# Performance work log

Hardware: AMD Instinct MI355X
Metric: run time of the kernel (lower is better)

Reference implementation:

```python
import jax, jax.numpy as jnp
import numpy as np

B, M, H, E = 1, 2048, 16, 128
D = H * E          # 2048, model dim
C = 4 * D          # 8192, FFN dim
F = E
G = D
J = D


def setup_inputs() -> dict:
    key = jax.random.key(0)
    k_in, k_wv, k_wk, k_wq, k_wz, k_ffa, k_ffb = jax.random.split(key, 7)
    scale = 0.01
    return {
        "I_in": jax.random.normal(k_in, (B, M, D), dtype=jnp.float32),
        "WV": jax.random.normal(k_wv, (H, E, D), dtype=jnp.float32) * scale,
        "WK": jax.random.normal(k_wk, (H, E, D), dtype=jnp.float32) * scale,
        "WQ": jax.random.normal(k_wq, (H, E, D), dtype=jnp.float32) * scale,
        "WZ": jax.random.normal(k_wz, (H, F, G), dtype=jnp.float32) * scale,
        "WFFA": jax.random.normal(k_ffa, (G, C), dtype=jnp.float32) * scale,
        "WFFB": jax.random.normal(k_ffb, (C, J), dtype=jnp.float32) * scale,
    }


def reference(I_in, WV, WK, WQ, WZ, WFFA, WFFB):
    # QKV projections: [B,M,D] x [H,E,D] -> [B,M,H,E]
    V = jnp.einsum('bmd,hed->bmhe', I_in, WV)
    K = jnp.einsum('bmd,hed->bmhe', I_in, WK)
    Q = jnp.einsum('bmd,hed->bmhe', I_in, WQ)
    # Attention scores [B,M,P,H]; NOTE: no 1/sqrt(E) scaling in the original.
    QK = jnp.einsum('bmhe,bphe->bmph', Q, K)
    # Softmax over keys (p axis = 2), matching torch.softmax(QK, dim=2)
    QK_softmax = jax.nn.softmax(QK, axis=2)
    # Attention output [B,M,H,E]
    AV = jnp.einsum('bmph,bphe->bmhe', QK_softmax, V)
    # Output projection [B,M,G]
    Z = jnp.einsum('bmhf,hfg->bmg', AV, WZ)
    # FFN (no nonlinearity in the original workload)
    FFA = jnp.einsum('bmg,gc->bmc', Z, WFFA)
    FFB = jnp.einsum('bmc,cj->bmj', FFA, WFFB)
    return FFB
```

## Files before the change

### kernel.cpp

```cpp
#include <hip/hip_runtime.h>
#include <hip/hip_bf16.h>
#include <math.h>


typedef __bf16 bf16_t;
typedef __bf16 bf16x8 __attribute__((ext_vector_type(8)));
typedef float  f32x4  __attribute__((ext_vector_type(4)));

#define AS1 __attribute__((address_space(1)))
#define AS3 __attribute__((address_space(3)))

__device__ __forceinline__ void load16_lds(const bf16_t* g, bf16_t* l) {
    __builtin_amdgcn_global_load_lds((AS1 void*)g, (AS3 void*)l, 16, 0, 0);
}

__device__ __forceinline__ void stageA_half(const bf16_t* __restrict__ Ab, int lda,
                                            int k0, int h, bf16_t* slot,
                                            int w, int lane)
{
    #pragma unroll
    for (int j = 0; j < 2; ++j) {
        const int prw = j * 64 + w * 8;
        const int p   = prw + (lane >> 3);
        const int lr  = (p >> 6) * 128 + h * 64 + (p & 63);
        const int lc  = (lane & 7) ^ (p & 7);
        load16_lds(Ab + (long long)lr * lda + k0 + lc * 8, slot + prw * 64);
    }
}
__device__ __forceinline__ void stageB_half(const bf16_t* __restrict__ Bb, int ldb,
                                            int k0, int h, bf16_t* slot,
                                            int w, int lane)
{
    #pragma unroll
    for (int j = 0; j < 2; ++j) {
        const int prw = j * 64 + w * 8;
        const int p   = prw + (lane >> 3);
        const int lr  = (p >> 5) * 64 + h * 32 + (p & 31);
        const int lc  = (lane & 7) ^ (p & 7);
        load16_lds(Bb + (long long)lr * ldb + k0 + lc * 8, slot + prw * 64);
    }
}

#define LOADAF(DST, SL)                                                        \
  _Pragma("unroll") for (int ks = 0; ks < 2; ++ks)                             \
  _Pragma("unroll") for (int mi = 0; mi < 4; ++mi)                             \
      DST[ks][mi] = *(const bf16x8*)&(SL)[(wm * 64 + mi * 16 + c15) * 64 +     \
                      (((ks * 4 + q4) ^ (c15 & 7)) * 8)];

#define LOADBV(DST, SL)                                                        \
  _Pragma("unroll") for (int ks = 0; ks < 2; ++ks)                             \
  _Pragma("unroll") for (int nj = 0; nj < 2; ++nj)                             \
      DST[ks][nj] = *(const bf16x8*)&(SL)[(wn * 32 + nj * 16 + c15) * 64 +     \
                      (((ks * 4 + q4) ^ (c15 & 7)) * 8)];

#define MFMA8(R0, C0)                                                          \
  _Pragma("unroll") for (int ks = 0; ks < 2; ++ks)                             \
  _Pragma("unroll") for (int mi = 0; mi < 4; ++mi)                             \
  _Pragma("unroll") for (int nj = 0; nj < 2; ++nj)                             \
      acc[(R0) + mi][(C0) + nj] = __builtin_amdgcn_mfma_f32_16x16x32_bf16(     \
          af[ks][mi], bv[ks][nj], acc[(R0) + mi][(C0) + nj], 0, 0, 0);

#define VMW(N)  asm volatile("s_waitcnt vmcnt(" #N ")" ::: "memory")
#define BAR()   __builtin_amdgcn_s_barrier()

#define PHASE8(RDS, STGS, GATE, R0, C0)                                        \
  RDS;                                                                         \
  STGS;                                                                        \
  GATE;                                                                        \
  __builtin_amdgcn_s_barrier();                                                \
  asm volatile("s_waitcnt lgkmcnt(0)" ::: "memory");                           \
  __builtin_amdgcn_sched_barrier(0);                                           \
  __builtin_amdgcn_s_setprio(1);                                               \
  MFMA8(R0, C0);                                                               \
  __builtin_amdgcn_s_setprio(0);                                               \
  __builtin_amdgcn_s_barrier();

template<typename TOUT>
__global__ __launch_bounds__(512, 2)
void gemm256p_bt(const bf16_t* __restrict__ A, const bf16_t* __restrict__ B,
                 TOUT* __restrict__ Cc, int Kdim,
                 int lda, int ldb, int ldc,
                 long long ab, long long bb, long long cb,
                 int ct_z, bf16_t* __restrict__ ctc, int ldct)
{
    __shared__ __attribute__((aligned(16))) bf16_t As4[4][128 * 64];
    __shared__ __attribute__((aligned(16))) bf16_t Bs4[4][128 * 64];

    const int z = blockIdx.z;
    A  += (long long)z * ab;
    B  += (long long)z * bb;
    Cc += (long long)z * cb;

    const int bm = blockIdx.y * 256;
    const int bn = blockIdx.x * 256;
    const int t = threadIdx.x, lane = t & 63, w = t >> 6;
    const int wm = w >> 2, wn = w & 3;
    const int q4 = lane >> 4, c15 = lane & 15;

    const bf16_t* Ab = A + (long long)bm * lda;
    const bf16_t* Bb = B + (long long)bn * ldb;

    f32x4  acc[8][4] = {};
    bf16x8 af[2][4];
    bf16x8 bv[2][2];

    stageB_half(Bb, ldb, 0,  0, Bs4[0], w, lane);
    stageA_half(Ab, lda, 0,  1, As4[1], w, lane);
    stageA_half(Ab, lda, 0,  0, As4[0], w, lane);
    stageB_half(Bb, ldb, 0,  1, Bs4[1], w, lane);
    stageB_half(Bb, ldb, 64, 0, Bs4[2], w, lane);
    stageA_half(Ab, lda, 64, 1, As4[3], w, lane);
    VMW(4);
    BAR();

    const int NT = Kdim >> 6;
    const int kcap = (NT - 1) << 6;

    for (int i = 0; i < NT / 2; ++i) {
        const int u  = 2 * i;
        const int k1 = (u + 1) << 6;
        int k2 = (u + 2) << 6; if (k2 > kcap) k2 = kcap;
        int k3 = (u + 3) << 6; if (k3 > kcap) k3 = kcap;
        PHASE8( LOADAF(af, As4[0]); LOADBV(bv, Bs4[0]),
                stageA_half(Ab, lda, k1, 0, As4[2], w, lane), ((void)0), 0, 0)
        PHASE8( LOADAF(af, As4[1]),
                stageB_half(Bb, ldb, k1, 1, Bs4[3], w, lane), ((void)0), 4, 0)
        PHASE8( LOADBV(bv, Bs4[1]),
                stageB_half(Bb, ldb, k2, 0, Bs4[0], w, lane), ((void)0), 4, 2)
        PHASE8( LOADAF(af, As4[0]),
                stageA_half(Ab, lda, k2, 1, As4[1], w, lane), VMW(4), 0, 2)
        PHASE8( LOADAF(af, As4[2]); LOADBV(bv, Bs4[2]),
                stageA_half(Ab, lda, k2, 0, As4[0], w, lane), ((void)0), 0, 0)
        PHASE8( LOADAF(af, As4[3]),
                stageB_half(Bb, ldb, k2, 1, Bs4[1], w, lane), ((void)0), 4, 0)
        PHASE8( LOADBV(bv, Bs4[3]),
                stageB_half(Bb, ldb, k3, 0, Bs4[2], w, lane), ((void)0), 4, 2)
        PHASE8( LOADAF(af, As4[2]),
                stageA_half(Ab, lda, k3, 1, As4[3], w, lane), VMW(4), 0, 2)
    }
    VMW(0);

    const int rb = q4 * 4;
    if (z == ct_z) {
        #pragma unroll
        for (int mi = 0; mi < 8; ++mi) {
            const long long mb = bm + wm * 128 + mi * 16 + rb;
            #pragma unroll
            for (int nj = 0; nj < 4; ++nj) {
                const long long n = bn + wn * 64 + nj * 16 + c15;
                union { bf16_t b[4]; unsigned long long u; } o;
                #pragma unroll
                for (int r = 0; r < 4; ++r) o.b[r] = (bf16_t)acc[mi][nj][r];
                *(unsigned long long*)(ctc + n * ldct + mb) = o.u;
            }
        }
    } else {
        #pragma unroll
        for (int mi = 0; mi < 8; ++mi) {
            #pragma unroll
            for (int r = 0; r < 4; ++r) {
                const long long m = bm + wm * 128 + mi * 16 + rb + r;
                TOUT* crow = Cc + m * ldc + bn + wn * 64 + c15;
                #pragma unroll
                for (int nj = 0; nj < 4; ++nj)
                    crow[nj * 16] = (TOUT)acc[mi][nj][r];
            }
        }
    }
}

template<typename TOUT, bool ATOMIC>
__global__ __launch_bounds__(256)
void gemm_bt(const bf16_t* __restrict__ A, const bf16_t* __restrict__ B,
             TOUT* __restrict__ Cc, int Mdim, int Ndim, int Kdim,
             int lda, int ldb, int ldc,
             long long ab, long long bb, long long cb,
             int ct_z, bf16_t* __restrict__ ctc, int ldct)
{
    __shared__ bf16_t Ash[128 * 32];
    __shared__ bf16_t Bsh[128 * 32];

    const int z = blockIdx.z;
    A  += (long long)z * ab;
    B  += (long long)z * bb;
    Cc += (long long)z * cb;

    const int bm = blockIdx.y * 128;
    const int bn = blockIdx.x * 128;
    const int t  = threadIdx.x;
    const int lane = t & 63;
    const int w    = t >> 6;

    const int wm = (w & 1) * 64;
    const int wn = (w >> 1) * 64;

    const int sub = lane >> 2;
    const int seg = lane & 3;

    const bf16_t* Ag0 = A + (long long)(bm + w * 32 + sub) * lda + seg * 8;
    const bf16_t* Ag1 = Ag0 + 16LL * lda;
    const bf16_t* Bg0 = B + (long long)(bn + w * 32 + sub) * ldb + seg * 8;
    const bf16_t* Bg1 = Bg0 + 16LL * ldb;

    bf16_t* Al0 = &Ash[(w * 2 + 0) * 512];
    bf16_t* Al1 = &Ash[(w * 2 + 1) * 512];
    bf16_t* Bl0 = &Bsh[(w * 2 + 0) * 512];
    bf16_t* Bl1 = &Bsh[(w * 2 + 1) * 512];

    const int col  = lane & 15;
    const int koff = (lane >> 4) * 8;

    f32x4 acc[4][4] = {};

    for (int k0 = 0; k0 < Kdim; k0 += 32) {
        load16_lds(Ag0 + k0, Al0);
        load16_lds(Ag1 + k0, Al1);
        load16_lds(Bg0 + k0, Bl0);
        load16_lds(Bg1 + k0, Bl1);
        __syncthreads();

        bf16x8 afr[4], bfr[4];
        #pragma unroll
        for (int mi = 0; mi < 4; ++mi)
            afr[mi] = *(const bf16x8*)&Ash[(wm + mi * 16 + col) * 32 + koff];
        #pragma unroll
        for (int nj = 0; nj < 4; ++nj)
            bfr[nj] = *(const bf16x8*)&Bsh[(wn + nj * 16 + col) * 32 + koff];
        #pragma unroll
        for (int mi = 0; mi < 4; ++mi)
            #pragma unroll
            for (int nj = 0; nj < 4; ++nj)
                acc[mi][nj] = __builtin_amdgcn_mfma_f32_16x16x32_bf16(
                    afr[mi], bfr[nj], acc[mi][nj], 0, 0, 0);
        __syncthreads();
    }

    const int rbase = (lane >> 4) * 4;
    if (z == ct_z) {
        #pragma unroll
        for (int mi = 0; mi < 4; ++mi) {
            const long long mb = bm + wm + mi * 16 + rbase;
            #pragma unroll
            for (int nj = 0; nj < 4; ++nj) {
                const long long n = bn + wn + nj * 16 + col;
                union { bf16_t b[4]; unsigned long long u; } o;
                #pragma unroll
                for (int r = 0; r < 4; ++r) o.b[r] = (bf16_t)acc[mi][nj][r];
                *(unsigned long long*)(ctc + n * ldct + mb) = o.u;
            }
        }
    } else {
        #pragma unroll
        for (int mi = 0; mi < 4; ++mi) {
            #pragma unroll
            for (int r = 0; r < 4; ++r) {
                long long m = bm + wm + mi * 16 + rbase + r;
                TOUT* crow = Cc + m * ldc + bn + wn + col;
                #pragma unroll
                for (int nj = 0; nj < 4; ++nj) {
                    if constexpr (ATOMIC)
                        atomicAdd(&crow[nj * 16], (float)acc[mi][nj][r]);
                    else
                        crow[nj * 16] = (TOUT)acc[mi][nj][r];
                }
            }
        }
    }
}

__global__ __launch_bounds__(256, 2)
void flash_attn(const bf16_t* __restrict__ Q, const bf16_t* __restrict__ K,
                const bf16_t* __restrict__ VT, bf16_t* __restrict__ O,
                int M, int D)
{
    __shared__ bf16_t Kt[64 * 128];
    __shared__ bf16_t Vt[128 * 64];
    __shared__ bf16_t Pl[4 * 16 * 88];

    const int t = threadIdx.x, lane = t & 63, w = t >> 6;
    const int q4 = lane >> 4;
    const int c  = lane & 15;
    const int bm = blockIdx.x * 64;
    const int hE = blockIdx.y * 128;

    bf16x8 af_q[4];
    {
        const bf16_t* qrow = Q + (long long)(bm + w * 16 + c) * D + hE + q4 * 8;
        #pragma unroll
        for (int ks = 0; ks < 4; ++ks)
            af_q[ks] = *(const bf16x8*)(qrow + ks * 32);
    }

    f32x4 acc_o[8] = {};
    float m_i[4] = {-INFINITY, -INFINITY, -INFINITY, -INFINITY};
    float l_i[4] = {0.f, 0.f, 0.f, 0.f};

    bf16_t* Pw = &Pl[w * 16 * 88];

    for (int p0 = 0; p0 < M; p0 += 64) {
        #pragma unroll
        for (int j = 0; j < 4; ++j) {
            int krow = w * 16 + j * 4;
            load16_lds(K + (long long)(p0 + krow + q4) * D + hE + ((c ^ (j * 4 + q4)) * 8),
                       &Kt[krow * 128]);
            int vrow = w * 32 + j * 8;
            load16_lds(VT + (long long)(hE + vrow + (lane >> 3)) * M + p0
                          + (((lane & 7) ^ (lane >> 3)) * 8),
                       &Vt[vrow * 64]);
        }
        __syncthreads();

        f32x4 acc_s[4] = {};
        #pragma unroll
        for (int ks = 0; ks < 4; ++ks) {
            #pragma unroll
            for (int nj = 0; nj < 4; ++nj) {
                int row = nj * 16 + c;
                bf16x8 bk = *(const bf16x8*)&Kt[row * 128 + (((ks * 4 + q4) ^ c) * 8)];
                acc_s[nj] = __builtin_amdgcn_mfma_f32_16x16x32_bf16(
                    af_q[ks], bk, acc_s[nj], 0, 0, 0);
            }
        }

        float mt[4], alpha[4], rs[4];
        #pragma unroll
        for (int r = 0; r < 4; ++r) {
            float v = fmaxf(fmaxf(acc_s[0][r], acc_s[1][r]),
                            fmaxf(acc_s[2][r], acc_s[3][r]));
            #pragma unroll
            for (int off = 1; off < 16; off <<= 1)
                v = fmaxf(v, __shfl_xor(v, off));
            mt[r] = v;
        }
        #pragma unroll
        for (int r = 0; r < 4; ++r) {
            float mn = fmaxf(m_i[r], mt[r]);
            alpha[r] = __expf(m_i[r] - mn);
            m_i[r] = mn;
            rs[r] = 0.f;
        }
        #pragma unroll
        for (int nj = 0; nj < 4; ++nj)
            #pragma unroll
            for (int r = 0; r < 4; ++r) {
                float p = __expf(acc_s[nj][r] - m_i[r]);
                rs[r] += p;
                Pw[(q4 * 4 + r) * 88 + nj * 16 + c] = (bf16_t)p;
            }
        #pragma unroll
        for (int r = 0; r < 4; ++r) {
            float v = rs[r];
            #pragma unroll
            for (int off = 1; off < 16; off <<= 1)
                v += __shfl_xor(v, off);
            l_i[r] = alpha[r] * l_i[r] + v;
        }
        #pragma unroll
        for (int nj = 0; nj < 8; ++nj)
            #pragma unroll
            for (int r = 0; r < 4; ++r)
                acc_o[nj][r] *= alpha[r];
        __syncthreads();

        #pragma unroll
        for (int ks = 0; ks < 2; ++ks) {
            bf16x8 ap = *(const bf16x8*)&Pw[c * 88 + ks * 32 + q4 * 8];
            #pragma unroll
            for (int nj = 0; nj < 8; ++nj) {
                int row = nj * 16 + c;
                bf16x8 bvv = *(const bf16x8*)&Vt[row * 64 + (((ks * 4 + q4) ^ (c & 7)) * 8)];
                acc_o[nj] = __builtin_amdgcn_mfma_f32_16x16x32_bf16(
                    ap, bvv, acc_o[nj], 0, 0, 0);
            }
        }
        __syncthreads();
    }

    float inv[4];
    #pragma unroll
    for (int r = 0; r < 4; ++r) inv[r] = 1.0f / l_i[r];
    #pragma unroll
    for (int nj = 0; nj < 8; ++nj)
        #pragma unroll
        for (int r = 0; r < 4; ++r)
            O[(long long)(bm + w * 16 + q4 * 4 + r) * D + hE + nj * 16 + c] =
                (bf16_t)(acc_o[nj][r] * inv[r]);
}

__global__ __launch_bounds__(256)
void cast4_bf16(const float* __restrict__ s0, const float* __restrict__ s1,
                const float* __restrict__ s2, const float* __restrict__ s3,
                bf16_t* __restrict__ d0, long long seg, long long n)
{
    const float* src = (blockIdx.y == 0) ? s0 : (blockIdx.y == 1) ? s1
                     : (blockIdx.y == 2) ? s2 : s3;
    bf16_t* dst = d0 + (long long)blockIdx.y * seg;
    long long i = ((long long)blockIdx.x * 256 + threadIdx.x) * 4;
    if (i >= n) return;
    float4 v = *(const float4*)(src + i);
    union { bf16_t b[4]; unsigned long long u; } o;
    o.b[0] = (bf16_t)v.x; o.b[1] = (bf16_t)v.y;
    o.b[2] = (bf16_t)v.z; o.b[3] = (bf16_t)v.w;
    *(unsigned long long*)(dst + i) = o.u;
}

__global__ __launch_bounds__(256)
void transpose_to_bf16(const float* __restrict__ in, bf16_t* __restrict__ out,
                       int rows, int cols)
{
    __shared__ bf16_t tile[32][33];
    const int r0 = blockIdx.y * 32, c0 = blockIdx.x * 32;
    const int tx = threadIdx.x & 31, ty = threadIdx.x >> 5;
    #pragma unroll
    for (int i = 0; i < 4; ++i) {
        int r = ty + i * 8;
        tile[r][tx] = (bf16_t)in[(long long)(r0 + r) * cols + c0 + tx];
    }
    __syncthreads();
    #pragma unroll
    for (int i = 0; i < 4; ++i) {
        int r = ty + i * 8;
        out[(long long)(c0 + r) * rows + r0 + tx] = tile[tx][r];
    }
}

__global__ __launch_bounds__(256)
void reduce4_f32(const float* __restrict__ p, float* __restrict__ out,
                 long long n)
{
    long long i = ((long long)blockIdx.x * 256 + threadIdx.x) * 4;
    if (i >= n) return;
    float4 a = *(const float4*)(p + i);
    float4 b = *(const float4*)(p + n + i);
    float4 c = *(const float4*)(p + 2 * n + i);
    float4 d = *(const float4*)(p + 3 * n + i);
    float4 o;
    o.x = a.x + b.x + c.x + d.x;
    o.y = a.y + b.y + c.y + d.y;
    o.z = a.z + b.z + c.z + d.z;
    o.w = a.w + b.w + c.w + d.w;
    *(float4*)(out + i) = o;
}

extern "C" void kernel_launch(void* const* d_in, const int* in_sizes, int n_in,
                              void* d_out, int out_size, void* d_ws, size_t ws_size,
                              hipStream_t stream)
{
    const float* I    = (const float*)d_in[0];
    const float* WV   = (const float*)d_in[1];
    const float* WK   = (const float*)d_in[2];
    const float* WQ   = (const float*)d_in[3];
    const float* WZ   = (const float*)d_in[4];
    const float* WFFA = (const float*)d_in[5];
    const float* WFFB = (const float*)d_in[6];
    float* out = (float*)d_out;

    const int M = 2048, D = 2048, C = 8192;
    const long long MD = (long long)M * D;
    const size_t MiB = 1024 * 1024;

    char* base = (char*)d_ws;
    bf16_t* bI     = (bf16_t*)(base + 0 * MiB);
    bf16_t* bWQ    = (bf16_t*)(base + 8 * MiB);
    bf16_t* bWK    = (bf16_t*)(base + 16 * MiB);
    bf16_t* bWV    = (bf16_t*)(base + 24 * MiB);
    bf16_t* bQ     = (bf16_t*)(base + 32 * MiB);
    bf16_t* bK     = (bf16_t*)(base + 40 * MiB);
    bf16_t* bVT    = (bf16_t*)(base + 48 * MiB);
    bf16_t* bAV    = (bf16_t*)(base + 56 * MiB);
    bf16_t* bZ     = (bf16_t*)(base + 64 * MiB);
    bf16_t* bWZT   = (bf16_t*)(base + 72 * MiB);
    bf16_t* bWFFAT = (bf16_t*)(base + 80 * MiB);
    bf16_t* bWFFBT = (bf16_t*)(base + 112 * MiB);
    bf16_t* bFFA   = (bf16_t*)(base + 0 * MiB);
    float*  pF     = (float*)(base + 32 * MiB);

    const dim3 blk(256);
    const dim3 blk512(512);

    cast4_bf16<<<dim3(MD / 1024, 4), blk, 0, stream>>>(I, WQ, WK, WV, bI, MD, MD);
    transpose_to_bf16<<<dim3(D / 32, D / 32), blk, 0, stream>>>(WZ,   bWZT,   D, D);
    transpose_to_bf16<<<dim3(C / 32, D / 32), blk, 0, stream>>>(WFFA, bWFFAT, D, C);
    transpose_to_bf16<<<dim3(D / 32, C / 32), blk, 0, stream>>>(WFFB, bWFFBT, C, D);

    gemm256p_bt<bf16_t><<<dim3(8, 8, 3), blk512, 0, stream>>>(
        bI, bWQ, bQ, D, D, D, D, 0, MD, MD, 2, bVT, M);

    flash_attn<<<dim3(M / 64, 16), blk, 0, stream>>>(bQ, bK, bVT, bAV, M, D);

    gemm_bt<bf16_t, false><<<dim3(16, 16, 1), blk, 0, stream>>>(
        bAV, bWZT, bZ, M, D, D, D, D, D, 0, 0, 0, -1, nullptr, 0);

    gemm256p_bt<bf16_t><<<dim3(32, 8, 1), blk512, 0, stream>>>(
        bZ, bWFFAT, bFFA, D, D, D, C, 0, 0, 0, -1, nullptr, 0);

    gemm256p_bt<float><<<dim3(8, 8, 4), blk512, 0, stream>>>(
        bFFA, bWFFBT, pF, 2048, C, C, D, 2048, 2048, MD, -1, nullptr, 0);

    reduce4_f32<<<dim3((int)(MD / 1024)), blk, 0, stream>>>(pF, out, MD);
}
```

Before: 603.0 us.

## Double-buffer K/V tiles in flash attention with async LDS prefetch

```diff
diff --git a/kernel.cpp b/kernel.cpp
--- a/kernel.cpp
+++ b/kernel.cpp
@@ -61,6 +61,7 @@
           af[ks][mi], bv[ks][nj], acc[(R0) + mi][(C0) + nj], 0, 0, 0);
 
 #define VMW(N)  asm volatile("s_waitcnt vmcnt(" #N ")" ::: "memory")
+#define LGKM0() asm volatile("s_waitcnt lgkmcnt(0)" ::: "memory")
 #define BAR()   __builtin_amdgcn_s_barrier()
 
 #define PHASE8(RDS, STGS, GATE, R0, C0)                                        \
@@ -273,8 +274,8 @@
                 const bf16_t* __restrict__ VT, bf16_t* __restrict__ O,
                 int M, int D)
 {
-    __shared__ bf16_t Kt[64 * 128];
-    __shared__ bf16_t Vt[128 * 64];
+    __shared__ bf16_t Kt[2][64 * 128];
+    __shared__ bf16_t Vt[2][128 * 64];
     __shared__ bf16_t Pl[4 * 16 * 88];
 
     const int t = threadIdx.x, lane = t & 63, w = t >> 6;
@@ -297,30 +298,43 @@
 
     bf16_t* Pw = &Pl[w * 16 * 88];
 
-    for (int p0 = 0; p0 < M; p0 += 64) {
-        #pragma unroll
-        for (int j = 0; j < 4; ++j) {
-            int krow = w * 16 + j * 4;
-            load16_lds(K + (long long)(p0 + krow + q4) * D + hE + ((c ^ (j * 4 + q4)) * 8),
-                       &Kt[krow * 128]);
-            int vrow = w * 32 + j * 8;
-            load16_lds(VT + (long long)(hE + vrow + (lane >> 3)) * M + p0
-                          + (((lane & 7) ^ (lane >> 3)) * 8),
-                       &Vt[vrow * 64]);
-        }
-        __syncthreads();
+    const int NT = M >> 6;
+
+    #define FA_STAGE(P0, B)                                                    \
+      _Pragma("unroll")                                                        \
+      for (int j = 0; j < 4; ++j) {                                            \
+          int krow = w * 16 + j * 4;                                           \
+          load16_lds(K + (long long)((P0) + krow + q4) * D + hE +              \
+                         ((c ^ (j * 4 + q4)) * 8),                             \
+                     &Kt[B][krow * 128]);                                      \
+          int vrow = w * 32 + j * 8;                                           \
+          load16_lds(VT + (long long)(hE + vrow + (lane >> 3)) * M + (P0) +    \
+                         (((lane & 7) ^ (lane >> 3)) * 8),                     \
+                     &Vt[B][vrow * 64]);                                       \
+      }
+
+    FA_STAGE(0, 0)
+
+    for (int ti = 0; ti < NT; ++ti) {
+        const int cur = ti & 1;
+        const int pn = (ti + 1 < NT) ? (ti + 1) * 64 : ti * 64;
+        FA_STAGE(pn, cur ^ 1)
+        VMW(8);
+        BAR();
 
         f32x4 acc_s[4] = {};
+        __builtin_amdgcn_s_setprio(1);
         #pragma unroll
         for (int ks = 0; ks < 4; ++ks) {
             #pragma unroll
             for (int nj = 0; nj < 4; ++nj) {
                 int row = nj * 16 + c;
-                bf16x8 bk = *(const bf16x8*)&Kt[row * 128 + (((ks * 4 + q4) ^ c) * 8)];
+                bf16x8 bk = *(const bf16x8*)&Kt[cur][row * 128 + (((ks * 4 + q4) ^ c) * 8)];
                 acc_s[nj] = __builtin_amdgcn_mfma_f32_16x16x32_bf16(
                     af_q[ks], bk, acc_s[nj], 0, 0, 0);
             }
         }
+        __builtin_amdgcn_s_setprio(0);
 
         float mt[4], alpha[4], rs[4];
         #pragma unroll
@@ -360,21 +374,26 @@
             #pragma unroll
             for (int r = 0; r < 4; ++r)
                 acc_o[nj][r] *= alpha[r];
-        __syncthreads();
-
+
+        LGKM0();
+        __builtin_amdgcn_sched_barrier(0);
+
+        __builtin_amdgcn_s_setprio(1);
         #pragma unroll
         for (int ks = 0; ks < 2; ++ks) {
             bf16x8 ap = *(const bf16x8*)&Pw[c * 88 + ks * 32 + q4 * 8];
             #pragma unroll
             for (int nj = 0; nj < 8; ++nj) {
                 int row = nj * 16 + c;
-                bf16x8 bvv = *(const bf16x8*)&Vt[row * 64 + (((ks * 4 + q4) ^ (c & 7)) * 8)];
+                bf16x8 bvv = *(const bf16x8*)&Vt[cur][row * 64 + (((ks * 4 + q4) ^ (c & 7)) * 8)];
                 acc_o[nj] = __builtin_amdgcn_mfma_f32_16x16x32_bf16(
                     ap, bvv, acc_o[nj], 0, 0, 0);
             }
         }
-        __syncthreads();
-    }
+        __builtin_amdgcn_s_setprio(0);
+        BAR();
+    }
+    VMW(0);
 
     float inv[4];
     #pragma unroll
@@ -385,6 +404,7 @@
         for (int r = 0; r < 4; ++r)
             O[(long long)(bm + w * 16 + q4 * 4 + r) * D + hE + nj * 16 + c] =
                 (bf16_t)(acc_o[nj][r] * inv[r]);
+    #undef FA_STAGE
 }
 
 __global__ __launch_bounds__(256)
```

After: 599.4 us. About the same (-0.6%).
